# Performance work log

Measured on AMD Instinct MI355X. Metric: run time of the kernel, lower is better.

Reference implementation:

```python
import jax, jax.numpy as jnp
import numpy as np

NEG_SLOPE = 0.2  # PyG GATConv default LeakyReLU slope
NUM_GRAPHS = 64


def gat_layer(x, src, dst, W, a_src, a_dst, b, concat):
    """PyG GATConv (eval mode, add_self_loops=True).
    x: [N, F_in]; W: [F_in, H*C]; a_src,a_dst: [H, C]; b: [H*C] or [C].
    """
    N = x.shape[0]
    H, C = a_src.shape
    h = (x @ W).reshape(N, H, C)                      # [N, H, C]
    # add self-loops
    loop = jnp.arange(N, dtype=src.dtype)
    s = jnp.concatenate([src, loop])                  # [E+N]
    d = jnp.concatenate([dst, loop])
    al_s = jnp.einsum('nhc,hc->nh', h, a_src)         # [N, H]
    al_d = jnp.einsum('nhc,hc->nh', h, a_dst)
    e = jax.nn.leaky_relu(al_s[s] + al_d[d], NEG_SLOPE)   # [E+N, H]
    # segment softmax over incoming edges per destination node
    m = jax.ops.segment_max(e, d, num_segments=N)     # [N, H]
    ex = jnp.exp(e - m[d])
    denom = jax.ops.segment_sum(ex, d, num_segments=N)
    alpha = ex / denom[d]                             # [E+N, H]
    msg = h[s] * alpha[:, :, None]                    # [E+N, H, C]
    out = jax.ops.segment_sum(msg, d, num_segments=N) # [N, H, C]
    out = out.reshape(N, H * C) if concat else out.mean(axis=1)
    return out + b


def setup_inputs() -> dict:
    key = jax.random.key(0)
    ks = jax.random.split(key, 16)
    N, E, F_in, Hid, Out = 50000, 800000, 128, 64, 10
    x = jax.random.normal(ks[0], (N, F_in), dtype=jnp.float32)
    edge_index = jax.random.randint(ks[1], (2, E), 0, N, dtype=jnp.int32)
    batch = jnp.sort(jax.random.randint(ks[2], (N,), 0, NUM_GRAPHS, dtype=jnp.int32))

    def glorot(k, shape):
        fan = shape[0] + shape[-1]
        return jax.random.normal(k, shape, dtype=jnp.float32) * np.sqrt(2.0 / fan)

    H1 = 8
    params = dict(
        W1=glorot(ks[3], (F_in, H1 * Hid)), a1_src=glorot(ks[4], (H1, Hid)),
        a1_dst=glorot(ks[5], (H1, Hid)), b1=jnp.zeros((H1 * Hid,), jnp.float32),
        W2=glorot(ks[6], (H1 * Hid, Hid)), a2_src=glorot(ks[7], (1, Hid)),
        a2_dst=glorot(ks[8], (1, Hid)), b2=jnp.zeros((Hid,), jnp.float32),
        W3=glorot(ks[9], (Hid, Hid)), a3_src=glorot(ks[10], (1, Hid)),
        a3_dst=glorot(ks[11], (1, Hid)), b3=jnp.zeros((Hid,), jnp.float32),
        fc_W=glorot(ks[12], (Hid, Out)), fc_b=jnp.zeros((Out,), jnp.float32),
    )
    return dict(x=x, edge_index=edge_index, batch=batch, **params)


def reference(x, edge_index, batch,
              W1, a1_src, a1_dst, b1,
              W2, a2_src, a2_dst, b2,
              W3, a3_src, a3_dst, b3,
              fc_W, fc_b):
    src, dst = edge_index[0], edge_index[1]
    # dropout is a no-op in eval mode
    h = jax.nn.elu(gat_layer(x, src, dst, W1, a1_src, a1_dst, b1, concat=True))
    h = jax.nn.elu(gat_layer(h, src, dst, W2, a2_src, a2_dst, b2, concat=False))
    h = jax.nn.elu(gat_layer(h, src, dst, W3, a3_src, a3_dst, b3, concat=False))
    # global mean pool over graphs
    sums = jax.ops.segment_sum(h, batch, num_segments=NUM_GRAPHS)
    cnts = jax.ops.segment_sum(jnp.ones((h.shape[0], 1), h.dtype), batch,
                               num_segments=NUM_GRAPHS)
    pooled = sums / jnp.maximum(cnts, 1.0)
    return pooled @ fc_W + fc_b
```

## Files before the change

kernel.cpp:

```cpp
#include <hip/hip_runtime.h>
#include <hip/hip_bf16.h>
#include <cstdint>

#define NEG_SLOPE 0.2f

typedef __attribute__((ext_vector_type(8))) short bf16x8;
typedef __attribute__((ext_vector_type(4))) float f32x4;

__device__ __forceinline__ float bf2f(uint32_t u) {
  union { float f; uint32_t i; } v;
  v.i = u << 16;
  return v.f;
}
__device__ __forceinline__ float lo16(uint32_t u) {
  union { float f; uint32_t i; } v;
  v.i = u << 16;
  return v.f;
}
__device__ __forceinline__ float hi16(uint32_t u) {
  union { float f; uint32_t i; } v;
  v.i = u & 0xffff0000u;
  return v.f;
}
__device__ __forceinline__ ushort f2bf(float f) {
  union { float f; uint32_t i; } v;
  v.f = f;
  uint32_t r = v.i + 0x7FFF + ((v.i >> 16) & 1);
  return (ushort)(r >> 16);
}

__global__ void prep_kernel(const float4* __restrict__ x,
                            uint2* __restrict__ x_bf, int n_x4,
                            const float* __restrict__ W1,
                            ushort* __restrict__ W1T,
                            const float* __restrict__ W2,
                            ushort* __restrict__ W2T,
                            const float* __restrict__ W3,
                            ushort* __restrict__ W3T,
                            const int* __restrict__ dst, int* __restrict__ cnt,
                            float* __restrict__ sums, int E) {
  int i = blockIdx.x * 256 + threadIdx.x;
  const int r0 = n_x4;
  const int r1 = r0 + 512 * 128;
  const int r2 = r1 + 64 * 512;
  const int r3 = r2 + 64 * 64;
  const int r4 = r3 + E;
  const int r5 = r4 + 64 * 64;
  if (i < r0) {
    float4 v = x[i];
    uint2 o;
    o.x = (uint32_t)f2bf(v.x) | ((uint32_t)f2bf(v.y) << 16);
    o.y = (uint32_t)f2bf(v.z) | ((uint32_t)f2bf(v.w) << 16);
    x_bf[i] = o;
  } else if (i < r1) {
    int idx = i - r0;
    int n = idx >> 7, k = idx & 127;
    W1T[idx] = f2bf(W1[(size_t)k * 512 + n]);
  } else if (i < r2) {
    int idx = i - r1;
    int n = idx >> 9, k = idx & 511;
    W2T[idx] = f2bf(W2[(size_t)k * 64 + n]);
  } else if (i < r3) {
    int idx = i - r2;
    int n = idx >> 6, k = idx & 63;
    W3T[idx] = f2bf(W3[(size_t)k * 64 + n]);
  } else if (i < r4) {
    atomicAdd(&cnt[dst[i - r3]], 1);
  } else if (i < r5) {
    sums[i - r4] = 0.f;
  }
}

__global__ __launch_bounds__(256) void gemm1_al(
    const ushort* __restrict__ A, const ushort* __restrict__ BT,
    ushort* __restrict__ C, const float* __restrict__ a1s,
    const float* __restrict__ a1d, float* __restrict__ al_s,
    float* __restrict__ al_d, int M) {
  const int K = 128;
  const int wave = threadIdx.x >> 6;
  const int lane = threadIdx.x & 63;
  const int rt = blockIdx.y * 4 + wave;
  const int r0 = rt * 16;
  if (r0 >= M) return;
  const int bx = blockIdx.x;
  const int n0 = bx * 128;
  const int l15 = lane & 15, q = lane >> 4;
  const ushort* Ap = A + (size_t)(r0 + l15) * K + q * 8;
  f32x4 acc[8] = {};
  for (int k0 = 0; k0 < K; k0 += 32) {
    bf16x8 a = *(const bf16x8*)(Ap + k0);
#pragma unroll
    for (int j = 0; j < 8; ++j) {
      const bf16x8 b =
          *(const bf16x8*)(BT + (size_t)(n0 + j * 16 + l15) * K + q * 8 + k0);
      acc[j] = __builtin_amdgcn_mfma_f32_16x16x32_bf16(a, b, acc[j], 0, 0, 0);
    }
  }
#pragma unroll
  for (int j = 0; j < 8; ++j)
#pragma unroll
    for (int r = 0; r < 4; ++r) {
      int row = r0 + q * 4 + r;
      C[(size_t)row * 512 + n0 + j * 16 + l15] = f2bf(acc[j][r]);
    }
  float als_p[2][4] = {{0.f}};
  float ald_p[2][4] = {{0.f}};
#pragma unroll
  for (int j = 0; j < 8; ++j) {
    int head = bx * 2 + (j >> 2);
    int cih = (j & 3) * 16 + l15;
    float wsc = a1s[head * 64 + cih];
    float wdc = a1d[head * 64 + cih];
#pragma unroll
    for (int r = 0; r < 4; ++r) {
      als_p[j >> 2][r] = fmaf(acc[j][r], wsc, als_p[j >> 2][r]);
      ald_p[j >> 2][r] = fmaf(acc[j][r], wdc, ald_p[j >> 2][r]);
    }
  }
#pragma unroll
  for (int g = 0; g < 2; ++g)
#pragma unroll
    for (int r = 0; r < 4; ++r) {
      float vs = als_p[g][r], vd = ald_p[g][r];
#pragma unroll
      for (int off = 1; off < 16; off <<= 1) {
        vs += __shfl_xor(vs, off);
        vd += __shfl_xor(vd, off);
      }
      if (l15 == 0) {
        int row = r0 + q * 4 + r;
        al_s[(size_t)row * 8 + bx * 2 + g] = vs;
        al_d[(size_t)row * 8 + bx * 2 + g] = vd;
      }
    }
}

__global__ __launch_bounds__(256) void gemm_n64_al(
    const ushort* __restrict__ A, const ushort* __restrict__ BT,
    ushort* __restrict__ C, const float* __restrict__ asrc,
    const float* __restrict__ adst, float* __restrict__ al_s,
    float* __restrict__ al_d, int M, int K) {
  const int wave = threadIdx.x >> 6;
  const int lane = threadIdx.x & 63;
  const int rt = blockIdx.y * 4 + wave;
  const int r0 = rt * 16;
  if (r0 >= M) return;
  const int l15 = lane & 15, q = lane >> 4;
  const ushort* Ap = A + (size_t)(r0 + l15) * K + q * 8;
  f32x4 acc[4] = {};
  for (int k0 = 0; k0 < K; k0 += 32) {
    bf16x8 a = *(const bf16x8*)(Ap + k0);
#pragma unroll
    for (int j = 0; j < 4; ++j) {
      const bf16x8 b =
          *(const bf16x8*)(BT + (size_t)(j * 16 + l15) * K + q * 8 + k0);
      acc[j] = __builtin_amdgcn_mfma_f32_16x16x32_bf16(a, b, acc[j], 0, 0, 0);
    }
  }
#pragma unroll
  for (int j = 0; j < 4; ++j)
#pragma unroll
    for (int r = 0; r < 4; ++r) {
      int row = r0 + q * 4 + r;
      C[(size_t)row * 64 + j * 16 + l15] = f2bf(acc[j][r]);
    }
  float als_p[4] = {0.f, 0.f, 0.f, 0.f};
  float ald_p[4] = {0.f, 0.f, 0.f, 0.f};
#pragma unroll
  for (int j = 0; j < 4; ++j) {
    float wsc = asrc[j * 16 + l15];
    float wdc = adst[j * 16 + l15];
#pragma unroll
    for (int r = 0; r < 4; ++r) {
      als_p[r] = fmaf(acc[j][r], wsc, als_p[r]);
      ald_p[r] = fmaf(acc[j][r], wdc, ald_p[r]);
    }
  }
#pragma unroll
  for (int r = 0; r < 4; ++r) {
    float vs = als_p[r], vd = ald_p[r];
#pragma unroll
    for (int off = 1; off < 16; off <<= 1) {
      vs += __shfl_xor(vs, off);
      vd += __shfl_xor(vd, off);
    }
    if (l15 == 0) {
      int row = r0 + q * 4 + r;
      al_s[row] = vs;
      al_d[row] = vd;
    }
  }
}

__global__ void scan_block(const int* __restrict__ in, int* __restrict__ out,
                           int* __restrict__ bsum, int n) {
  __shared__ int sm[256];
  int gid = blockIdx.x * 256 + threadIdx.x;
  int v = (gid < n) ? in[gid] : 0;
  sm[threadIdx.x] = v;
  __syncthreads();
  for (int off = 1; off < 256; off <<= 1) {
    int t = (threadIdx.x >= off) ? sm[threadIdx.x - off] : 0;
    __syncthreads();
    sm[threadIdx.x] += t;
    __syncthreads();
  }
  if (gid < n) out[gid] = sm[threadIdx.x];
  if (threadIdx.x == 255) bsum[blockIdx.x] = sm[255];
}

__global__ void scan_final2(const int* __restrict__ inc,
                            const int* __restrict__ bsum,
                            int* __restrict__ indptr, int* __restrict__ fill,
                            int n) {
  __shared__ int sm[256];
  const int t = threadIdx.x, bx = blockIdx.x;
  sm[t] = (t < bx) ? bsum[t] : 0;
  __syncthreads();
  for (int off = 128; off; off >>= 1) {
    if (t < off) sm[t] += sm[t + off];
    __syncthreads();
  }
  const int prefix = sm[0];
  int gid = bx * 256 + t;
  if (gid < n) {
    int val = inc[gid] + prefix;
    indptr[gid + 1] = val;
    fill[gid + 1] = val;
  }
  if (gid == 0) {
    indptr[0] = 0;
    fill[0] = 0;
  }
}

__global__ void scatter_kernel(const int* __restrict__ src,
                               const int* __restrict__ dst,
                               int* __restrict__ fill,
                               int* __restrict__ csr_src, int E) {
  int e = blockIdx.x * 256 + threadIdx.x;
  if (e < E) {
    int pos = atomicAdd(&fill[dst[e]], 1);
    csr_src[pos] = src[e];
  }
}

__global__ __launch_bounds__(256) void attn1_kernel(
    const int* __restrict__ indptr, const int* __restrict__ csr_src,
    const float* __restrict__ al_s, const float* __restrict__ al_d,
    const ushort* __restrict__ h1, const float* __restrict__ b1,
    ushort* __restrict__ out1, int Nn) {
  const int w = (blockIdx.x * 256 + threadIdx.x) >> 6;
  const int l = threadIdx.x & 63;
  if (w >= Nn) return;
  const int d = w;
  const int start = indptr[d];
  const int deg = indptr[d + 1] - start;
  const int total = deg + 1;
  const int head = l >> 3;
  const int hh = l & 7;
  const float ald_c = al_d[(size_t)d * 8 + hh];

  float acc[8] = {0.f, 0.f, 0.f, 0.f, 0.f, 0.f, 0.f, 0.f};
  float den = 0.f;
  const ushort* h1l = h1 + l * 8;

  int s_p = d;
  float a_p = 0.f;
  if (head < total) {
    s_p = (head < deg) ? csr_src[start + head] : d;
    a_p = al_s[(size_t)s_p * 8 + hh];
  }

  for (int e0 = 0; e0 < total; e0 += 8) {
    const int el = e0 + head;
    const int s_j = s_p;
    float v = a_p + ald_c;
    v = fmaxf(v, NEG_SLOPE * v);
    const float u = (el < total) ? __expf(v) : 0.f;

    int sv[8];
#pragma unroll
    for (int e = 0; e < 8; ++e) sv[e] = __shfl(s_j, e * 8);
    uint4 uu[8];
#pragma unroll
    for (int e = 0; e < 8; ++e)
      uu[e] = *(const uint4*)(h1l + (size_t)sv[e] * 512);

    den += u;
    const int eln = el + 8;
    if (eln < total) {
      s_p = (eln < deg) ? csr_src[start + eln] : d;
      a_p = al_s[(size_t)s_p * 8 + hh];
    } else {
      s_p = d;
      a_p = 0.f;
    }

    float au[8];
#pragma unroll
    for (int e = 0; e < 8; ++e) au[e] = __shfl(u, e * 8 + head);
#pragma unroll
    for (int e = 0; e < 8; ++e) {
      acc[0] = fmaf(au[e], lo16(uu[e].x), acc[0]);
      acc[1] = fmaf(au[e], hi16(uu[e].x), acc[1]);
      acc[2] = fmaf(au[e], lo16(uu[e].y), acc[2]);
      acc[3] = fmaf(au[e], hi16(uu[e].y), acc[3]);
      acc[4] = fmaf(au[e], lo16(uu[e].z), acc[4]);
      acc[5] = fmaf(au[e], hi16(uu[e].z), acc[5]);
      acc[6] = fmaf(au[e], lo16(uu[e].w), acc[6]);
      acc[7] = fmaf(au[e], hi16(uu[e].w), acc[7]);
    }
  }
  den += __shfl_xor(den, 8);
  den += __shfl_xor(den, 16);
  den += __shfl_xor(den, 32);
  const float inv = 1.f / __shfl(den, head);

  const float4 bb0 = *(const float4*)(b1 + l * 8);
  const float4 bb1 = *(const float4*)(b1 + l * 8 + 4);
  float o[8];
  o[0] = acc[0] * inv + bb0.x;
  o[1] = acc[1] * inv + bb0.y;
  o[2] = acc[2] * inv + bb0.z;
  o[3] = acc[3] * inv + bb0.w;
  o[4] = acc[4] * inv + bb1.x;
  o[5] = acc[5] * inv + bb1.y;
  o[6] = acc[6] * inv + bb1.z;
  o[7] = acc[7] * inv + bb1.w;
#pragma unroll
  for (int k = 0; k < 8; ++k) o[k] = (o[k] > 0.f) ? o[k] : __expf(o[k]) - 1.f;
  uint4 st;
  st.x = (uint32_t)f2bf(o[0]) | ((uint32_t)f2bf(o[1]) << 16);
  st.y = (uint32_t)f2bf(o[2]) | ((uint32_t)f2bf(o[3]) << 16);
  st.z = (uint32_t)f2bf(o[4]) | ((uint32_t)f2bf(o[5]) << 16);
  st.w = (uint32_t)f2bf(o[6]) | ((uint32_t)f2bf(o[7]) << 16);
  *(uint4*)(out1 + (size_t)d * 512 + l * 8) = st;
}

__global__ __launch_bounds__(256) void attn_h1_kernel(
    const int* __restrict__ indptr, const int* __restrict__ csr_src,
    const float* __restrict__ al_s, const float* __restrict__ al_d,
    const ushort* __restrict__ hin, const float* __restrict__ bias,
    ushort* __restrict__ outp, int Nn) {
  const int w = (blockIdx.x * 256 + threadIdx.x) >> 6;
  const int l = threadIdx.x & 63;
  if (w >= Nn) return;
  const int d = w;
  const int start = indptr[d];
  const int deg = indptr[d + 1] - start;
  const int total = deg + 1;
  const int t = l >> 3;
  const int c8 = l & 7;
  const float ald = al_d[d];
  const ushort* hl = hin + c8 * 8;

  float acc[8] = {0.f, 0.f, 0.f, 0.f, 0.f, 0.f, 0.f, 0.f};
  float den = 0.f;

  for (int e0 = 0; e0 < total; e0 += 64) {
    const int e = e0 + l;
    int s_l = d;
    float u_l = 0.f;
    if (e < total) {
      s_l = (e < deg) ? csr_src[start + e] : d;
      float v = al_s[s_l] + ald;
      v = fmaxf(v, NEG_SLOPE * v);
      u_l = __expf(v);
      den += u_l;
    }
    const int ne = min(64, total - e0);
    int su0 = __shfl(s_l, t);
    float uv0 = __shfl(u_l, t);
    uint4 h0 = *(const uint4*)(hl + (size_t)su0 * 64);
    int j = 0;
    for (; j + 8 < ne; j += 8) {
      const int su1 = __shfl(s_l, j + 8 + t);
      const float uv1 = __shfl(u_l, j + 8 + t);
      const uint4 h1v = *(const uint4*)(hl + (size_t)su1 * 64);
      acc[0] = fmaf(uv0, lo16(h0.x), acc[0]);
      acc[1] = fmaf(uv0, hi16(h0.x), acc[1]);
      acc[2] = fmaf(uv0, lo16(h0.y), acc[2]);
      acc[3] = fmaf(uv0, hi16(h0.y), acc[3]);
      acc[4] = fmaf(uv0, lo16(h0.z), acc[4]);
      acc[5] = fmaf(uv0, hi16(h0.z), acc[5]);
      acc[6] = fmaf(uv0, lo16(h0.w), acc[6]);
      acc[7] = fmaf(uv0, hi16(h0.w), acc[7]);
      uv0 = uv1;
      h0 = h1v;
    }
    acc[0] = fmaf(uv0, lo16(h0.x), acc[0]);
    acc[1] = fmaf(uv0, hi16(h0.x), acc[1]);
    acc[2] = fmaf(uv0, lo16(h0.y), acc[2]);
    acc[3] = fmaf(uv0, hi16(h0.y), acc[3]);
    acc[4] = fmaf(uv0, lo16(h0.z), acc[4]);
    acc[5] = fmaf(uv0, hi16(h0.z), acc[5]);
    acc[6] = fmaf(uv0, lo16(h0.w), acc[6]);
    acc[7] = fmaf(uv0, hi16(h0.w), acc[7]);
  }
#pragma unroll
  for (int k = 0; k < 8; ++k) {
    acc[k] += __shfl_xor(acc[k], 8);
    acc[k] += __shfl_xor(acc[k], 16);
    acc[k] += __shfl_xor(acc[k], 32);
  }
#pragma unroll
  for (int off = 32; off; off >>= 1) den += __shfl_xor(den, off);
  const float inv = 1.f / den;
  if (l < 8) {
    float o[8];
#pragma unroll
    for (int k = 0; k < 8; ++k) {
      float v = acc[k] * inv + bias[l * 8 + k];
      o[k] = (v > 0.f) ? v : __expf(v) - 1.f;
    }
    uint4 st;
    st.x = (uint32_t)f2bf(o[0]) | ((uint32_t)f2bf(o[1]) << 16);
    st.y = (uint32_t)f2bf(o[2]) | ((uint32_t)f2bf(o[3]) << 16);
    st.z = (uint32_t)f2bf(o[4]) | ((uint32_t)f2bf(o[5]) << 16);
    st.w = (uint32_t)f2bf(o[6]) | ((uint32_t)f2bf(o[7]) << 16);
    *(uint4*)(outp + (size_t)d * 64 + l * 8) = st;
  }
}

__global__ __launch_bounds__(256) void pool_fc_kernel(
    const ushort* __restrict__ out3, const int* __restrict__ batch, int Nn,
    const float* __restrict__ fcW, const float* __restrict__ fcb,
    float* __restrict__ out) {
  __shared__ int bnds[2];
  __shared__ float sm[4 * 64];
  __shared__ float pm[64];
  const int tid = threadIdx.x;
  const int g = blockIdx.x;
  if (tid < 2) {
    int target = g + tid;
    int lo = 0, hi = Nn;
    while (lo < hi) {
      int mid = (lo + hi) >> 1;
      if (batch[mid] < target) lo = mid + 1; else hi = mid;
    }
    bnds[tid] = lo;
  }
  __syncthreads();
  const int lb = bnds[0], ub = bnds[1];

  const int ro = tid >> 3, c8 = tid & 7;
  float acc[8] = {0.f, 0.f, 0.f, 0.f, 0.f, 0.f, 0.f, 0.f};
  for (int r = lb + ro; r < ub; r += 32) {
    const uint4 hh4 = *(const uint4*)(out3 + (size_t)r * 64 + c8 * 8);
    acc[0] += lo16(hh4.x);
    acc[1] += hi16(hh4.x);
    acc[2] += lo16(hh4.y);
    acc[3] += hi16(hh4.y);
    acc[4] += lo16(hh4.z);
    acc[5] += hi16(hh4.z);
    acc[6] += lo16(hh4.w);
    acc[7] += hi16(hh4.w);
  }
#pragma unroll
  for (int k = 0; k < 8; ++k) {
    acc[k] += __shfl_xor(acc[k], 8);
    acc[k] += __shfl_xor(acc[k], 16);
    acc[k] += __shfl_xor(acc[k], 32);
  }
  const int wv = tid >> 6, ll = tid & 63;
  if (ll < 8) {
#pragma unroll
    for (int k = 0; k < 8; ++k) sm[wv * 64 + ll * 8 + k] = acc[k];
  }
  __syncthreads();
  if (tid < 64) {
    float tot = sm[tid] + sm[64 + tid] + sm[128 + tid] + sm[192 + tid];
    pm[tid] = tot / fmaxf((float)(ub - lb), 1.f);
  }
  __syncthreads();
  if (tid < 10) {
    float a = fcb[tid];
    for (int c = 0; c < 64; ++c) a = fmaf(pm[c], fcW[c * 10 + tid], a);
    out[g * 10 + tid] = a;
  }
}

extern "C" void kernel_launch(void* const* d_in, const int* in_sizes, int n_in,
                              void* d_out, int out_size, void* d_ws,
                              size_t ws_size, hipStream_t stream) {
  const float* x = (const float*)d_in[0];
  const int* ei = (const int*)d_in[1];
  const int* batch = (const int*)d_in[2];
  const float* W1 = (const float*)d_in[3];
  const float* a1s = (const float*)d_in[4];
  const float* a1d = (const float*)d_in[5];
  const float* b1 = (const float*)d_in[6];
  const float* W2 = (const float*)d_in[7];
  const float* a2s = (const float*)d_in[8];
  const float* a2d = (const float*)d_in[9];
  const float* b2 = (const float*)d_in[10];
  const float* W3 = (const float*)d_in[11];
  const float* a3s = (const float*)d_in[12];
  const float* a3d = (const float*)d_in[13];
  const float* b3 = (const float*)d_in[14];
  const float* fcW = (const float*)d_in[15];
  const float* fcb = (const float*)d_in[16];
  float* out = (float*)d_out;

  const int N = in_sizes[0] / 128;
  const int E = in_sizes[1] / 2;
  const int* srcp = ei;
  const int* dstp = ei + E;

  char* ws = (char*)d_ws;
  size_t off = 0;
  auto alloc = [&](size_t bytes) -> void* {
    off = (off + 255) & ~(size_t)255;
    void* p = ws + off;
    off += bytes;
    return p;
  };
  ushort* x_bf = (ushort*)alloc((size_t)N * 128 * 2);
  ushort* W1T = (ushort*)alloc(512 * 128 * 2);
  ushort* W2T = (ushort*)alloc(64 * 512 * 2);
  ushort* W3T = (ushort*)alloc(64 * 64 * 2);
  ushort* h1 = (ushort*)alloc((size_t)N * 512 * 2);
  ushort* out1 = (ushort*)alloc((size_t)N * 512 * 2);
  float* al_s1 = (float*)alloc((size_t)N * 8 * 4);
  float* al_d1 = (float*)alloc((size_t)N * 8 * 4);
  float* al_s2 = (float*)alloc((size_t)N * 4);
  float* al_d2 = (float*)alloc((size_t)N * 4);
  float* al_s3 = (float*)alloc((size_t)N * 4);
  float* al_d3 = (float*)alloc((size_t)N * 4);
  int* cnt = (int*)alloc((size_t)N * 4);
  int* fill = (int*)alloc((size_t)(N + 1) * 4);
  int* indptr = (int*)alloc((size_t)(N + 1) * 4);
  int* csr = (int*)alloc((size_t)E * 4);
  int* incbuf = (int*)alloc((size_t)N * 4);
  int* bsum = (int*)alloc(1024 * 4);
  float* sums = (float*)alloc(64 * 64 * 4);

  ushort* h2 = h1;
  ushort* out2 = h1 + (size_t)N * 64;
  ushort* h3 = h1 + (size_t)2 * N * 64;
  ushort* out3 = h1 + (size_t)3 * N * 64;

  hipMemsetAsync(cnt, 0, (size_t)N * 4, stream);

  const int scan_blocks = (N + 255) / 256;
  const int row_blocks = (N / 16 + 3) / 4;

  const int n_x4 = N * 128 / 4;
  const int prep_total = n_x4 + 512 * 128 + 64 * 512 + 64 * 64 + E + 64 * 64;
  prep_kernel<<<(prep_total + 255) / 256, 256, 0, stream>>>(
      (const float4*)x, (uint2*)x_bf, n_x4, W1, W1T, W2, W2T, W3, W3T, dstp,
      cnt, sums, E);

  gemm1_al<<<dim3(4, row_blocks), 256, 0, stream>>>(x_bf, W1T, h1, a1s, a1d,
                                                    al_s1, al_d1, N);
  scan_block<<<scan_blocks, 256, 0, stream>>>(cnt, incbuf, bsum, N);
  scan_final2<<<scan_blocks, 256, 0, stream>>>(incbuf, bsum, indptr, fill, N);
  scatter_kernel<<<(E + 255) / 256, 256, 0, stream>>>(srcp, dstp, fill, csr, E);
  attn1_kernel<<<(N + 3) / 4, 256, 0, stream>>>(indptr, csr, al_s1, al_d1, h1,
                                                b1, out1, N);

  gemm_n64_al<<<dim3(1, row_blocks), 256, 0, stream>>>(out1, W2T, h2, a2s, a2d,
                                                       al_s2, al_d2, N, 512);
  attn_h1_kernel<<<(N + 3) / 4, 256, 0, stream>>>(indptr, csr, al_s2, al_d2, h2,
                                                  b2, out2, N);

  gemm_n64_al<<<dim3(1, row_blocks), 256, 0, stream>>>(out2, W3T, h3, a3s, a3d,
                                                       al_s3, al_d3, N, 64);
  attn_h1_kernel<<<(N + 3) / 4, 256, 0, stream>>>(indptr, csr, al_s3, al_d3, h3,
                                                  b3, out3, N);

  pool_fc_kernel<<<64, 256, 0, stream>>>(out3, batch, N, fcW, fcb, out);
}
```

Baseline: 502.5 us.

## Aggregate raw inputs per head before projecting layer one

```diff
diff --git a/kernel.cpp b/kernel.cpp
--- a/kernel.cpp
+++ b/kernel.cpp
@@ -38,14 +38,18 @@
                             const float* __restrict__ W3,
                             ushort* __restrict__ W3T,
                             const int* __restrict__ dst, int* __restrict__ cnt,
-                            float* __restrict__ sums, int E) {
+                            const float* __restrict__ a1s,
+                            const float* __restrict__ a1d,
+                            float* __restrict__ at_s, float* __restrict__ at_d,
+                            int E) {
   int i = blockIdx.x * 256 + threadIdx.x;
   const int r0 = n_x4;
   const int r1 = r0 + 512 * 128;
   const int r2 = r1 + 64 * 512;
   const int r3 = r2 + 64 * 64;
   const int r4 = r3 + E;
-  const int r5 = r4 + 64 * 64;
+  const int r5 = r4 + 1024;
+  const int r6 = r5 + 1024;
   if (i < r0) {
     float4 v = x[i];
     uint2 o;
@@ -67,72 +71,54 @@
   } else if (i < r4) {
     atomicAdd(&cnt[dst[i - r3]], 1);
   } else if (i < r5) {
-    sums[i - r4] = 0.f;
-  }
-}
-
-__global__ __launch_bounds__(256) void gemm1_al(
-    const ushort* __restrict__ A, const ushort* __restrict__ BT,
-    ushort* __restrict__ C, const float* __restrict__ a1s,
-    const float* __restrict__ a1d, float* __restrict__ al_s,
-    float* __restrict__ al_d, int M) {
-  const int K = 128;
-  const int wave = threadIdx.x >> 6;
-  const int lane = threadIdx.x & 63;
-  const int rt = blockIdx.y * 4 + wave;
-  const int r0 = rt * 16;
-  if (r0 >= M) return;
-  const int bx = blockIdx.x;
-  const int n0 = bx * 128;
-  const int l15 = lane & 15, q = lane >> 4;
-  const ushort* Ap = A + (size_t)(r0 + l15) * K + q * 8;
-  f32x4 acc[8] = {};
-  for (int k0 = 0; k0 < K; k0 += 32) {
-    bf16x8 a = *(const bf16x8*)(Ap + k0);
-#pragma unroll
-    for (int j = 0; j < 8; ++j) {
-      const bf16x8 b =
-          *(const bf16x8*)(BT + (size_t)(n0 + j * 16 + l15) * K + q * 8 + k0);
-      acc[j] = __builtin_amdgcn_mfma_f32_16x16x32_bf16(a, b, acc[j], 0, 0, 0);
-    }
-  }
-#pragma unroll
-  for (int j = 0; j < 8; ++j)
-#pragma unroll
-    for (int r = 0; r < 4; ++r) {
-      int row = r0 + q * 4 + r;
-      C[(size_t)row * 512 + n0 + j * 16 + l15] = f2bf(acc[j][r]);
-    }
-  float als_p[2][4] = {{0.f}};
-  float ald_p[2][4] = {{0.f}};
-#pragma unroll
-  for (int j = 0; j < 8; ++j) {
-    int head = bx * 2 + (j >> 2);
-    int cih = (j & 3) * 16 + l15;
-    float wsc = a1s[head * 64 + cih];
-    float wdc = a1d[head * 64 + cih];
-#pragma unroll
-    for (int r = 0; r < 4; ++r) {
-      als_p[j >> 2][r] = fmaf(acc[j][r], wsc, als_p[j >> 2][r]);
-      ald_p[j >> 2][r] = fmaf(acc[j][r], wdc, ald_p[j >> 2][r]);
-    }
-  }
-#pragma unroll
-  for (int g = 0; g < 2; ++g)
-#pragma unroll
-    for (int r = 0; r < 4; ++r) {
-      float vs = als_p[g][r], vd = ald_p[g][r];
-#pragma unroll
-      for (int off = 1; off < 16; off <<= 1) {
-        vs += __shfl_xor(vs, off);
-        vd += __shfl_xor(vd, off);
+    int idx = i - r4;
+    int k = idx >> 3, h = idx & 7;
+    float a = 0.f;
+    for (int c = 0; c < 64; ++c)
+      a = fmaf(W1[(size_t)k * 512 + h * 64 + c], a1s[h * 64 + c], a);
+    at_s[idx] = a;
+  } else if (i < r6) {
+    int idx = i - r5;
+    int k = idx >> 3, h = idx & 7;
+    float a = 0.f;
+    for (int c = 0; c < 64; ++c)
+      a = fmaf(W1[(size_t)k * 512 + h * 64 + c], a1d[h * 64 + c], a);
+    at_d[idx] = a;
+  }
+}
+
+__global__ __launch_bounds__(256) void algemm_kernel(
+    const ushort* __restrict__ x_bf, const float* __restrict__ at_s,
+    const float* __restrict__ at_d, float* __restrict__ al_s,
+    float* __restrict__ al_d, int Nn) {
+  const int n = blockIdx.x * 256 + threadIdx.x;
+  if (n >= Nn) return;
+  float as8[8] = {}, ad8[8] = {};
+  const ushort* xp = x_bf + (size_t)n * 128;
+  for (int k0 = 0; k0 < 128; k0 += 8) {
+    const uint4 xw = *(const uint4*)(xp + k0);
+    const uint32_t ww0 = xw.x, ww1 = xw.y, ww2 = xw.z, ww3 = xw.w;
+    float xv[8];
+    xv[0] = lo16(ww0); xv[1] = hi16(ww0);
+    xv[2] = lo16(ww1); xv[3] = hi16(ww1);
+    xv[4] = lo16(ww2); xv[5] = hi16(ww2);
+    xv[6] = lo16(ww3); xv[7] = hi16(ww3);
+#pragma unroll
+    for (int t = 0; t < 8; ++t) {
+      const int k = k0 + t;
+#pragma unroll
+      for (int h = 0; h < 8; ++h) {
+        as8[h] = fmaf(xv[t], at_s[k * 8 + h], as8[h]);
+        ad8[h] = fmaf(xv[t], at_d[k * 8 + h], ad8[h]);
       }
-      if (l15 == 0) {
-        int row = r0 + q * 4 + r;
-        al_s[(size_t)row * 8 + bx * 2 + g] = vs;
-        al_d[(size_t)row * 8 + bx * 2 + g] = vd;
-      }
-    }
+    }
+  }
+  float4* ps = (float4*)(al_s + (size_t)n * 8);
+  ps[0] = make_float4(as8[0], as8[1], as8[2], as8[3]);
+  ps[1] = make_float4(as8[4], as8[5], as8[6], as8[7]);
+  float4* pd = (float4*)(al_d + (size_t)n * 8);
+  pd[0] = make_float4(ad8[0], ad8[1], ad8[2], ad8[3]);
+  pd[1] = make_float4(ad8[4], ad8[5], ad8[6], ad8[7]);
 }
 
 __global__ __launch_bounds__(256) void gemm_n64_al(
@@ -192,6 +178,39 @@
   }
 }
 
+__global__ __launch_bounds__(256) void gemm1h_kernel(
+    const ushort* __restrict__ A, const ushort* __restrict__ BT,
+    const float* __restrict__ b1, ushort* __restrict__ C, int M) {
+  const int wave = threadIdx.x >> 6;
+  const int lane = threadIdx.x & 63;
+  const int rt = blockIdx.y * 4 + wave;
+  const int r0 = rt * 16;
+  if (r0 >= M) return;
+  const int hd = blockIdx.x;
+  const int l15 = lane & 15, q = lane >> 4;
+  const ushort* Ap = A + (size_t)(r0 + l15) * 1024 + hd * 128 + q * 8;
+  f32x4 acc[4] = {};
+  for (int k0 = 0; k0 < 128; k0 += 32) {
+    bf16x8 a = *(const bf16x8*)(Ap + k0);
+#pragma unroll
+    for (int j = 0; j < 4; ++j) {
+      const bf16x8 b = *(const bf16x8*)(BT + (size_t)(hd * 64 + j * 16 + l15) * 128 +
+                                        q * 8 + k0);
+      acc[j] = __builtin_amdgcn_mfma_f32_16x16x32_bf16(a, b, acc[j], 0, 0, 0);
+    }
+  }
+#pragma unroll
+  for (int j = 0; j < 4; ++j)
+#pragma unroll
+    for (int r = 0; r < 4; ++r) {
+      const int row = r0 + q * 4 + r;
+      const int col = hd * 64 + j * 16 + l15;
+      float v = acc[j][r] + b1[col];
+      v = (v > 0.f) ? v : __expf(v) - 1.f;
+      C[(size_t)row * 512 + col] = f2bf(v);
+    }
+}
+
 __global__ void scan_block(const int* __restrict__ in, int* __restrict__ out,
                            int* __restrict__ bsum, int n) {
   __shared__ int sm[256];
@@ -245,97 +264,105 @@
   }
 }
 
-__global__ __launch_bounds__(256) void attn1_kernel(
+__global__ __launch_bounds__(256) void attn1x_kernel(
     const int* __restrict__ indptr, const int* __restrict__ csr_src,
     const float* __restrict__ al_s, const float* __restrict__ al_d,
-    const ushort* __restrict__ h1, const float* __restrict__ b1,
-    ushort* __restrict__ out1, int Nn) {
+    const ushort* __restrict__ x_bf, ushort* __restrict__ agg, int Nn) {
+  __shared__ float u_sm[4][64 * 8];
+  __shared__ int s_sm[4][64];
+  const int wv = threadIdx.x >> 6;
+  const int l = threadIdx.x & 63;
   const int w = (blockIdx.x * 256 + threadIdx.x) >> 6;
-  const int l = threadIdx.x & 63;
   if (w >= Nn) return;
   const int d = w;
   const int start = indptr[d];
   const int deg = indptr[d + 1] - start;
   const int total = deg + 1;
-  const int head = l >> 3;
-  const int hh = l & 7;
-  const float ald_c = al_d[(size_t)d * 8 + hh];
-
-  float acc[8] = {0.f, 0.f, 0.f, 0.f, 0.f, 0.f, 0.f, 0.f};
+  const int h = l >> 3;
+  const int ks = l & 7;
+  const ushort* xcol = x_bf + ks * 16;
+  const float4 ad0 = *(const float4*)(al_d + (size_t)d * 8);
+  const float4 ad1 = *(const float4*)(al_d + (size_t)d * 8 + 4);
+
+  float acc[16] = {};
   float den = 0.f;
-  const ushort* h1l = h1 + l * 8;
-
-  int s_p = d;
-  float a_p = 0.f;
-  if (head < total) {
-    s_p = (head < deg) ? csr_src[start + head] : d;
-    a_p = al_s[(size_t)s_p * 8 + hh];
-  }
-
-  for (int e0 = 0; e0 < total; e0 += 8) {
-    const int el = e0 + head;
-    const int s_j = s_p;
-    float v = a_p + ald_c;
-    v = fmaxf(v, NEG_SLOPE * v);
-    const float u = (el < total) ? __expf(v) : 0.f;
-
-    int sv[8];
-#pragma unroll
-    for (int e = 0; e < 8; ++e) sv[e] = __shfl(s_j, e * 8);
-    uint4 uu[8];
-#pragma unroll
-    for (int e = 0; e < 8; ++e)
-      uu[e] = *(const uint4*)(h1l + (size_t)sv[e] * 512);
-
-    den += u;
-    const int eln = el + 8;
-    if (eln < total) {
-      s_p = (eln < deg) ? csr_src[start + eln] : d;
-      a_p = al_s[(size_t)s_p * 8 + hh];
-    } else {
-      s_p = d;
-      a_p = 0.f;
-    }
-
-    float au[8];
-#pragma unroll
-    for (int e = 0; e < 8; ++e) au[e] = __shfl(u, e * 8 + head);
-#pragma unroll
-    for (int e = 0; e < 8; ++e) {
-      acc[0] = fmaf(au[e], lo16(uu[e].x), acc[0]);
-      acc[1] = fmaf(au[e], hi16(uu[e].x), acc[1]);
-      acc[2] = fmaf(au[e], lo16(uu[e].y), acc[2]);
-      acc[3] = fmaf(au[e], hi16(uu[e].y), acc[3]);
-      acc[4] = fmaf(au[e], lo16(uu[e].z), acc[4]);
-      acc[5] = fmaf(au[e], hi16(uu[e].z), acc[5]);
-      acc[6] = fmaf(au[e], lo16(uu[e].w), acc[6]);
-      acc[7] = fmaf(au[e], hi16(uu[e].w), acc[7]);
-    }
-  }
-  den += __shfl_xor(den, 8);
-  den += __shfl_xor(den, 16);
-  den += __shfl_xor(den, 32);
-  const float inv = 1.f / __shfl(den, head);
-
-  const float4 bb0 = *(const float4*)(b1 + l * 8);
-  const float4 bb1 = *(const float4*)(b1 + l * 8 + 4);
-  float o[8];
-  o[0] = acc[0] * inv + bb0.x;
-  o[1] = acc[1] * inv + bb0.y;
-  o[2] = acc[2] * inv + bb0.z;
-  o[3] = acc[3] * inv + bb0.w;
-  o[4] = acc[4] * inv + bb1.x;
-  o[5] = acc[5] * inv + bb1.y;
-  o[6] = acc[6] * inv + bb1.z;
-  o[7] = acc[7] * inv + bb1.w;
-#pragma unroll
-  for (int k = 0; k < 8; ++k) o[k] = (o[k] > 0.f) ? o[k] : __expf(o[k]) - 1.f;
-  uint4 st;
-  st.x = (uint32_t)f2bf(o[0]) | ((uint32_t)f2bf(o[1]) << 16);
-  st.y = (uint32_t)f2bf(o[2]) | ((uint32_t)f2bf(o[3]) << 16);
-  st.z = (uint32_t)f2bf(o[4]) | ((uint32_t)f2bf(o[5]) << 16);
-  st.w = (uint32_t)f2bf(o[6]) | ((uint32_t)f2bf(o[7]) << 16);
-  *(uint4*)(out1 + (size_t)d * 512 + l * 8) = st;
+  float* usm = u_sm[wv];
+  int* ssm = s_sm[wv];
+
+  for (int e0 = 0; e0 < total; e0 += 64) {
+    const int e = e0 + l;
+    int s_l = d;
+    float u8[8] = {};
+    if (e < total) {
+      s_l = (e < deg) ? csr_src[start + e] : d;
+      const float4 s0 = *(const float4*)(al_s + (size_t)s_l * 8);
+      const float4 s1 = *(const float4*)(al_s + (size_t)s_l * 8 + 4);
+      float vv[8];
+      vv[0] = s0.x + ad0.x; vv[1] = s0.y + ad0.y;
+      vv[2] = s0.z + ad0.z; vv[3] = s0.w + ad0.w;
+      vv[4] = s1.x + ad1.x; vv[5] = s1.y + ad1.y;
+      vv[6] = s1.z + ad1.z; vv[7] = s1.w + ad1.w;
+#pragma unroll
+      for (int k = 0; k < 8; ++k) {
+        float v = fmaxf(vv[k], NEG_SLOPE * vv[k]);
+        u8[k] = __expf(v);
+      }
+    }
+    ssm[l] = s_l;
+    ((float4*)&usm[l * 8])[0] = make_float4(u8[0], u8[1], u8[2], u8[3]);
+    ((float4*)&usm[l * 8])[1] = make_float4(u8[4], u8[5], u8[6], u8[7]);
+
+    const int ne = min(64, total - e0);
+    const int NCh = (ne + 7) >> 3;
+    for (int c = 0; c < NCh; ++c) {
+      int sv[8];
+#pragma unroll
+      for (int t = 0; t < 8; ++t) sv[t] = ssm[c * 8 + t];
+      uint4 ra[8], rb[8];
+#pragma unroll
+      for (int t = 0; t < 8; ++t) {
+        const ushort* p = xcol + (size_t)sv[t] * 128;
+        ra[t] = *(const uint4*)p;
+        rb[t] = *(const uint4*)(p + 8);
+      }
+      float au[8];
+#pragma unroll
+      for (int t = 0; t < 8; ++t) au[t] = usm[(c * 8 + t) * 8 + h];
+#pragma unroll
+      for (int t = 0; t < 8; ++t) {
+        den += au[t];
+        acc[0] = fmaf(au[t], lo16(ra[t].x), acc[0]);
+        acc[1] = fmaf(au[t], hi16(ra[t].x), acc[1]);
+        acc[2] = fmaf(au[t], lo16(ra[t].y), acc[2]);
+        acc[3] = fmaf(au[t], hi16(ra[t].y), acc[3]);
+        acc[4] = fmaf(au[t], lo16(ra[t].z), acc[4]);
+        acc[5] = fmaf(au[t], hi16(ra[t].z), acc[5]);
+        acc[6] = fmaf(au[t], lo16(ra[t].w), acc[6]);
+        acc[7] = fmaf(au[t], hi16(ra[t].w), acc[7]);
+        acc[8] = fmaf(au[t], lo16(rb[t].x), acc[8]);
+        acc[9] = fmaf(au[t], hi16(rb[t].x), acc[9]);
+        acc[10] = fmaf(au[t], lo16(rb[t].y), acc[10]);
+        acc[11] = fmaf(au[t], hi16(rb[t].y), acc[11]);
+        acc[12] = fmaf(au[t], lo16(rb[t].z), acc[12]);
+        acc[13] = fmaf(au[t], hi16(rb[t].z), acc[13]);
+        acc[14] = fmaf(au[t], lo16(rb[t].w), acc[14]);
+        acc[15] = fmaf(au[t], hi16(rb[t].w), acc[15]);
+      }
+    }
+  }
+  const float inv = 1.f / den;
+  ushort* op = agg + (size_t)d * 1024 + l * 16;
+  uint4 st0, st1;
+  st0.x = (uint32_t)f2bf(acc[0] * inv) | ((uint32_t)f2bf(acc[1] * inv) << 16);
+  st0.y = (uint32_t)f2bf(acc[2] * inv) | ((uint32_t)f2bf(acc[3] * inv) << 16);
+  st0.z = (uint32_t)f2bf(acc[4] * inv) | ((uint32_t)f2bf(acc[5] * inv) << 16);
+  st0.w = (uint32_t)f2bf(acc[6] * inv) | ((uint32_t)f2bf(acc[7] * inv) << 16);
+  st1.x = (uint32_t)f2bf(acc[8] * inv) | ((uint32_t)f2bf(acc[9] * inv) << 16);
+  st1.y = (uint32_t)f2bf(acc[10] * inv) | ((uint32_t)f2bf(acc[11] * inv) << 16);
+  st1.z = (uint32_t)f2bf(acc[12] * inv) | ((uint32_t)f2bf(acc[13] * inv) << 16);
+  st1.w = (uint32_t)f2bf(acc[14] * inv) | ((uint32_t)f2bf(acc[15] * inv) << 16);
+  *(uint4*)op = st0;
+  *(uint4*)(op + 8) = st1;
 }
 
 __global__ __launch_bounds__(256) void attn_h1_kernel(
@@ -520,8 +547,11 @@
   ushort* W1T = (ushort*)alloc(512 * 128 * 2);
   ushort* W2T = (ushort*)alloc(64 * 512 * 2);
   ushort* W3T = (ushort*)alloc(64 * 64 * 2);
-  ushort* h1 = (ushort*)alloc((size_t)N * 512 * 2);
+  float* at_s = (float*)alloc(128 * 8 * 4);
+  float* at_d = (float*)alloc(128 * 8 * 4);
+  ushort* agg = (ushort*)alloc((size_t)N * 1024 * 2);
   ushort* out1 = (ushort*)alloc((size_t)N * 512 * 2);
+  ushort* hreg = (ushort*)alloc((size_t)4 * N * 64 * 2);
   float* al_s1 = (float*)alloc((size_t)N * 8 * 4);
   float* al_d1 = (float*)alloc((size_t)N * 8 * 4);
   float* al_s2 = (float*)alloc((size_t)N * 4);
@@ -534,12 +564,11 @@
   int* csr = (int*)alloc((size_t)E * 4);
   int* incbuf = (int*)alloc((size_t)N * 4);
   int* bsum = (int*)alloc(1024 * 4);
-  float* sums = (float*)alloc(64 * 64 * 4);
-
-  ushort* h2 = h1;
-  ushort* out2 = h1 + (size_t)N * 64;
-  ushort* h3 = h1 + (size_t)2 * N * 64;
-  ushort* out3 = h1 + (size_t)3 * N * 64;
+
+  ushort* h2 = hreg;
+  ushort* out2 = hreg + (size_t)N * 64;
+  ushort* h3 = hreg + (size_t)2 * N * 64;
+  ushort* out3 = hreg + (size_t)3 * N * 64;
 
   hipMemsetAsync(cnt, 0, (size_t)N * 4, stream);
 
@@ -547,18 +576,20 @@
   const int row_blocks = (N / 16 + 3) / 4;
 
   const int n_x4 = N * 128 / 4;
-  const int prep_total = n_x4 + 512 * 128 + 64 * 512 + 64 * 64 + E + 64 * 64;
+  const int prep_total = n_x4 + 512 * 128 + 64 * 512 + 64 * 64 + E + 2048;
   prep_kernel<<<(prep_total + 255) / 256, 256, 0, stream>>>(
       (const float4*)x, (uint2*)x_bf, n_x4, W1, W1T, W2, W2T, W3, W3T, dstp,
-      cnt, sums, E);
-
-  gemm1_al<<<dim3(4, row_blocks), 256, 0, stream>>>(x_bf, W1T, h1, a1s, a1d,
-                                                    al_s1, al_d1, N);
+      cnt, a1s, a1d, at_s, at_d, E);
+
+  algemm_kernel<<<(N + 255) / 256, 256, 0, stream>>>(x_bf, at_s, at_d, al_s1,
+                                                     al_d1, N);
   scan_block<<<scan_blocks, 256, 0, stream>>>(cnt, incbuf, bsum, N);
   scan_final2<<<scan_blocks, 256, 0, stream>>>(incbuf, bsum, indptr, fill, N);
   scatter_kernel<<<(E + 255) / 256, 256, 0, stream>>>(srcp, dstp, fill, csr, E);
-  attn1_kernel<<<(N + 3) / 4, 256, 0, stream>>>(indptr, csr, al_s1, al_d1, h1,
-                                                b1, out1, N);
+
+  attn1x_kernel<<<(N + 3) / 4, 256, 0, stream>>>(indptr, csr, al_s1, al_d1,
+                                                 x_bf, agg, N);
+  gemm1h_kernel<<<dim3(8, row_blocks), 256, 0, stream>>>(agg, W1T, b1, out1, N);
 
   gemm_n64_al<<<dim3(1, row_blocks), 256, 0, stream>>>(out1, W2T, h2, a2s, a2d,
                                                        al_s2, al_d2, N, 512);
```

Result: no change. 511.0 us (+1.7%).
